# Optimization experiments

Measured on AMD Instinct MI355X. Metric: run time of the kernel, lower is better.

## Reference

```python
import jax, jax.numpy as jnp
import numpy as np

NL = 4   # numLayers (modules are shared across layers)
H = 8    # numSignalHeads; contextAttention has embed_dim=1 with 1 head


def _ln(x, g, b, eps=1e-10):
    m = x.mean(-1, keepdims=True)
    v = ((x - m) ** 2).mean(-1, keepdims=True)
    return (x - m) / jnp.sqrt(v + eps) * g + b


def _forward(signalData, contextualData, Ws, bs, bn_g, bn_b,
             cWq, cWk, cWv, cbq, cbk, cbv, cbias_k, cbias_v, cWo, cbo,
             xWq, xWk, xWv, xbq, xbk, xbv, xbias_k, xbias_v, xWo, xbo,
             W1, b1, W2, b2, W3, b3,
             ln_ff_g, ln_ff_b, ln_cas_g, ln_cas_b, ln_fin_g, ln_fin_b):
    B, S, E = signalData.shape
    dh = E // H
    scale = float(1.0 / np.sqrt(dh))
    # synthesizeContext: Linear(C,18) + BatchNorm1d(18, track_running_stats=False -> batch stats)
    ec = contextualData @ Ws.T + bs                       # (B,18)
    mu = ec.mean(0)
    var = ((ec - mu) ** 2).mean(0)                        # biased var (PyTorch BN)
    ec = (ec - mu) / jnp.sqrt(var + 1e-5) * bn_g + bn_b
    ec = ec[:, :, None]                                   # (B,18,1)
    sig = signalData
    for _ in range(NL):
        # --- self-attention on context: embed_dim=1, 1 head (head_dim=1, scale=1), add_bias_kv ---
        q = ec @ cWq.T + cbq                              # (B,18,1)
        k = jnp.concatenate([ec @ cWk.T + cbk, jnp.broadcast_to(cbias_k, (B, 1, 1))], axis=1)
        v = jnp.concatenate([ec @ cWv.T + cbv, jnp.broadcast_to(cbias_v, (B, 1, 1))], axis=1)
        a = jax.nn.softmax(jnp.einsum('bqd,bkd->bqk', q, k), axis=-1)
        sa = jnp.einsum('bqk,bkd->bqd', a, v) @ cWo.T + cbo
        ec = ec + sa
        # --- cross-attention: query/value = LN(signal) (E), key = context (kdim=1), add_bias_kv ---
        ns = _ln(sig, ln_cas_g, ln_cas_b)
        q = (ns @ xWq.T + xbq).reshape(B, S, H, dh)
        k = jnp.concatenate([ec @ xWk.T + xbk, jnp.broadcast_to(xbias_k, (B, 1, E))], axis=1).reshape(B, S + 1, H, dh)
        v = jnp.concatenate([ns @ xWv.T + xbv, jnp.broadcast_to(xbias_v, (B, 1, E))], axis=1).reshape(B, S + 1, H, dh)
        a = jax.nn.softmax(jnp.einsum('bqhd,bkhd->bhqk', q, k) * scale, axis=-1)
        ca = jnp.einsum('bhqk,bkhd->bqhd', a, v).reshape(B, S, E) @ xWo.T + xbo
        sig = sig + ca
        # --- feed-forward: Linear->SiLU->Linear->SiLU->Linear->SiLU (dropout = identity in eval) ---
        nf = _ln(sig, ln_ff_g, ln_ff_b)
        ff = jax.nn.silu(jax.nn.silu(jax.nn.silu(nf @ W1.T + b1) @ W2.T + b2) @ W3.T + b3)
        sig = sig + ff
    return _ln(sig, ln_fin_g, ln_fin_b)


def setup_inputs() -> dict:
    key = jax.random.key(0)
    ks = iter(jax.random.split(key, 48))
    r = lambda *s: jax.random.normal(next(ks), s, dtype=jnp.float32) * 0.05
    B, S, E, C = 4096, 18, 256, 512
    return dict(
        signalData=jax.random.normal(next(ks), (B, S, E), dtype=jnp.float32),
        contextualData=jax.random.normal(next(ks), (B, C), dtype=jnp.float32),
        Ws=r(18, C), bs=r(18), bn_g=jnp.ones(18, jnp.float32), bn_b=jnp.zeros(18, jnp.float32),
        cWq=r(1, 1), cWk=r(1, 1), cWv=r(1, 1), cbq=r(1), cbk=r(1), cbv=r(1),
        cbias_k=r(1), cbias_v=r(1), cWo=r(1, 1), cbo=r(1),
        xWq=r(E, E), xWk=r(E, 1), xWv=r(E, E), xbq=r(E), xbk=r(E), xbv=r(E),
        xbias_k=r(E), xbias_v=r(E), xWo=r(E, E), xbo=r(E),
        W1=r(32, E), b1=r(32), W2=r(16, 32), b2=r(16), W3=r(E, 16), b3=r(E),
        ln_ff_g=jnp.ones(E, jnp.float32), ln_ff_b=jnp.zeros(E, jnp.float32),
        ln_cas_g=jnp.ones(E, jnp.float32), ln_cas_b=jnp.zeros(E, jnp.float32),
        ln_fin_g=jnp.ones(E, jnp.float32), ln_fin_b=jnp.zeros(E, jnp.float32),
    )


def reference(signalData, contextualData, Ws, bs, bn_g, bn_b,
              cWq, cWk, cWv, cbq, cbk, cbv, cbias_k, cbias_v, cWo, cbo,
              xWq, xWk, xWv, xbq, xbk, xbv, xbias_k, xbias_v, xWo, xbo,
              W1, b1, W2, b2, W3, b3,
              ln_ff_g, ln_ff_b, ln_cas_g, ln_cas_b, ln_fin_g, ln_fin_b):
    return _forward(signalData, contextualData, Ws, bs, bn_g, bn_b,
                    cWq, cWk, cWv, cbq, cbk, cbv, cbias_k, cbias_v, cWo, cbo,
                    xWq, xWk, xWv, xbq, xbk, xbv, xbias_k, xbias_v, xWo, xbo,
                    W1, b1, W2, b2, W3, b3,
                    ln_ff_g, ln_ff_b, ln_cas_g, ln_cas_b, ln_fin_g, ln_fin_b)
```

## Files before the change

### kernel.cpp

```cpp
#include <hip/hip_runtime.h>

typedef unsigned short u16;
typedef __attribute__((ext_vector_type(8))) short bf16x8;
typedef __attribute__((ext_vector_type(4))) float f32x4;
typedef __attribute__((ext_vector_type(4))) unsigned int u32x4;
typedef __attribute__((ext_vector_type(2))) unsigned int u32x2;

#define MROWS 36
#define SWZ(r,c) ((c) ^ (((r)&7)<<3))

__device__ inline u16 f2bf(float f){
  unsigned int u = __float_as_uint(f);
  return (u16)((u + 0x7fffu + ((u>>16)&1u)) >> 16);
}
__device__ inline unsigned int packbf(float a, float b){
  return (unsigned int)f2bf(a) | ((unsigned int)f2bf(b)<<16);
}
__device__ inline float bfloat_lo(unsigned int u){ return __uint_as_float(u<<16); }
__device__ inline float bfloat_hi(unsigned int u){ return __uint_as_float(u & 0xffff0000u); }
__device__ inline float bf2f(u16 h){ return __uint_as_float(((unsigned int)h)<<16); }
__device__ inline float wred(float v){
  #pragma unroll
  for (int m=1;m<64;m<<=1) v += __shfl_xor(v, m, 64);
  return v;
}
__device__ inline float silu_f(float x){ return x / (1.f + __expf(-x)); }
__device__ inline f32x4 mfma16(bf16x8 a, bf16x8 b, f32x4 c){
  return __builtin_amdgcn_mfma_f32_16x16x32_bf16(a, b, c, 0, 0, 0);
}

struct Params {
  const float *sigIn;
  const float *bn_g, *bn_b;
  const float *cWq,*cWk,*cWv,*cbq,*cbk,*cbv,*cbias_k,*cbias_v,*cWo,*cbo;
  const float *xbv, *xbias_v, *xbo;
  const float *b1,*b2,*b3;
  const float *g_cas,*b_cas,*g_ff,*b_ff,*g_fin,*b_fin;
  const u16 *Wv,*Wo,*Wq3,*W1b,*W2b,*W3p;
  const float *bias3, *ecr, *mu, *rstd;
  float *out;
};

__global__ void k_prep(const float* __restrict__ xWq, const float* __restrict__ xWk,
                       const float* __restrict__ xWv, const float* __restrict__ xWo,
                       const float* __restrict__ xbq, const float* __restrict__ xbk,
                       const float* __restrict__ xbias_k,
                       const float* __restrict__ W1, const float* __restrict__ W2,
                       const float* __restrict__ W3,
                       u16* Wv, u16* Wo, u16* Wq3, u16* W1b, u16* W2b, u16* W3p, float* bias3){
  const int gid = blockIdx.x*blockDim.x + threadIdx.x;
  const int gsz = gridDim.x*blockDim.x;
  for (int i=gid;i<65536;i+=gsz) Wv[i]=f2bf(xWv[i]);
  for (int i=gid;i<65536;i+=gsz) Wo[i]=f2bf(xWo[i]);
  for (int i=gid;i<8192;i+=gsz)  W1b[i]=f2bf(W1[i]);
  for (int i=gid;i<512;i+=gsz)   W2b[i]=f2bf(W2[i]);
  for (int i=gid;i<8192;i+=gsz){ int o=i>>5, k=i&31; W3p[i] = (k<16)? f2bf(W3[o*16+k]) : (u16)0; }
  for (int i=gid;i<8192;i+=gsz){
    int r=i>>8, c=i&255;
    u16 outv = 0;
    if (r<24){
      int h=r&7, sel=r>>3;
      const float* vec = sel==0? xWk : (sel==1? xbk : xbias_k);
      float s=0.f;
      for (int d=0;d<32;++d) s += xWq[(size_t)(h*32+d)*256+c]*vec[h*32+d];
      outv = f2bf(s);
    }
    Wq3[i]=outv;
  }
  for (int i=gid;i<24;i+=gsz){
    int h=i&7, sel=i>>3;
    const float* vec = sel==0? xWk : (sel==1? xbk : xbias_k);
    float s=0.f; for (int d=0;d<32;++d) s += xbq[h*32+d]*vec[h*32+d];
    bias3[i]=s;
  }
}

__global__ void k_ec(const float* __restrict__ ctx, const float* __restrict__ Ws,
                     const float* __restrict__ bs, float* __restrict__ ecr){
  const int wave = threadIdx.x>>6, lane = threadIdx.x&63;
  const int b = blockIdx.x*4 + wave;
  const float* c = ctx + (size_t)b*512 + lane*8;
  const float4 a0 = *(const float4*)c, a1 = *(const float4*)(c+4);
  float cv[8] = {a0.x,a0.y,a0.z,a0.w,a1.x,a1.y,a1.z,a1.w};
  #pragma unroll 1
  for (int j=0;j<18;++j){
    const float* w = Ws + j*512 + lane*8;
    const float4 w0 = *(const float4*)w, w1 = *(const float4*)(w+4);
    float s = cv[0]*w0.x + cv[1]*w0.y + cv[2]*w0.z + cv[3]*w0.w
            + cv[4]*w1.x + cv[5]*w1.y + cv[6]*w1.z + cv[7]*w1.w;
    s = wred(s);
    if (lane==0) ecr[(size_t)b*18 + j] = s + bs[j];
  }
}

__global__ void k_bn(const float* __restrict__ ecr, float* __restrict__ mu, float* __restrict__ rstd){
  __shared__ float red[256];
  const int tid = threadIdx.x;
  for (int j=0;j<18;++j){
    float s=0.f, s2=0.f;
    for (int b=tid;b<4096;b+=256){ float v = ecr[(size_t)b*18+j]; s+=v; s2+=v*v; }
    red[tid]=s; __syncthreads();
    for (int o=128;o>0;o>>=1){ if(tid<o) red[tid]+=red[tid+o]; __syncthreads(); }
    float S = red[0]; __syncthreads();
    red[tid]=s2; __syncthreads();
    for (int o=128;o>0;o>>=1){ if(tid<o) red[tid]+=red[tid+o]; __syncthreads(); }
    float S2 = red[0]; __syncthreads();
    if (tid==0){ float m = S*(1.f/4096.f); float v = S2*(1.f/4096.f) - m*m;
                 mu[j]=m; rstd[j]=rsqrtf(v+1e-5f); }
  }
}

__global__ __launch_bounds__(256, 2) void k_main(Params P){
  __shared__ __attribute__((aligned(16))) u16 s_sig[MROWS][256];
  __shared__ __attribute__((aligned(16))) u16 s_ns [MROWS][256];
  __shared__ __attribute__((aligned(16))) u16 s_v  [MROWS][256];
  __shared__ __attribute__((aligned(16))) u16 s_h1 [MROWS][32];
  __shared__ float s_qq[MROWS][24];
  __shared__ float s_ec[2][18];

  const int tid  = threadIdx.x;
  const int wave = tid >> 6;
  const int lane = tid & 63;
  const int lr   = lane & 15;
  const int lkg  = lane >> 4;
  const int kof  = lkg * 8;
  const int dr   = lkg * 4;
  const int b0   = blockIdx.x * 2;

  for (int idx = tid*8; idx < MROWS*256; idx += 256*8){
    const int row = idx >> 8, col = idx & 255;
    const float* src = P.sigIn + ((size_t)b0*18 + row)*256 + col;
    const float4 a = *(const float4*)src;
    const float4 b = *(const float4*)(src+4);
    u32x4 w;
    w[0]=packbf(a.x,a.y); w[1]=packbf(a.z,a.w);
    w[2]=packbf(b.x,b.y); w[3]=packbf(b.z,b.w);
    *(u32x4*)&s_sig[row][SWZ(row,col)] = w;
  }
  if (tid < 36){
    const int nb = tid/18, j = tid - nb*18;
    const float raw = P.ecr[(size_t)(b0+nb)*18 + j];
    s_ec[nb][j] = (raw - P.mu[j]) * P.rstd[j] * P.bn_g[j] + P.bn_b[j];
  }
  __syncthreads();

  auto ln_pass = [&](const float* g, const float* bvec){
    #pragma unroll 1
    for (int r = wave*9; r < wave*9+9; ++r){
      const int col = lane*4;
      const u32x2 raw = *(const u32x2*)&s_sig[r][SWZ(r,col)];
      const float x0 = bfloat_lo(raw[0]), x1 = bfloat_hi(raw[0]);
      const float x2 = bfloat_lo(raw[1]), x3 = bfloat_hi(raw[1]);
      const float m = wred(x0+x1+x2+x3)*(1.f/256.f);
      const float d0=x0-m, d1=x1-m, d2=x2-m, d3=x3-m;
      const float rs = rsqrtf(wred(d0*d0+d1*d1+d2*d2+d3*d3)*(1.f/256.f)+1e-10f);
      const float4 gv = *(const float4*)(g+col);
      const float4 bv = *(const float4*)(bvec+col);
      u32x2 o;
      o[0] = packbf(d0*rs*gv.x+bv.x, d1*rs*gv.y+bv.y);
      o[1] = packbf(d2*rs*gv.z+bv.z, d3*rs*gv.w+bv.w);
      *(u32x2*)&s_ns[r][SWZ(r,col)] = o;
    }
  };

  for (int layer = 0; layer < 4; ++layer){
    float newec = 0.f;
    if (tid < 36){
      const int nb = tid/18, i = tid - nb*18;
      const float cwq=P.cWq[0], cbq=P.cbq[0], cwk=P.cWk[0], cbk=P.cbk[0];
      const float cwv=P.cWv[0], cbv=P.cbv[0], ck1=P.cbias_k[0], cv1=P.cbias_v[0];
      const float cwo=P.cWo[0], cbo=P.cbo[0];
      const float qi = s_ec[nb][i]*cwq + cbq;
      float sc[19]; float mx = -1e30f;
      #pragma unroll
      for (int j=0;j<18;++j){ sc[j] = qi*(s_ec[nb][j]*cwk + cbk); mx = fmaxf(mx, sc[j]); }
      sc[18] = qi*ck1; mx = fmaxf(mx, sc[18]);
      float den=0.f, o=0.f;
      #pragma unroll
      for (int j=0;j<18;++j){ const float pp=__expf(sc[j]-mx); den+=pp; o+=pp*(s_ec[nb][j]*cwv+cbv); }
      const float pp=__expf(sc[18]-mx); den+=pp; o+=pp*cv1;
      newec = s_ec[nb][i] + (o/den)*cwo + cbo;
    }
    __syncthreads();
    if (tid < 36){ const int nb = tid/18; s_ec[nb][tid - nb*18] = newec; }

    ln_pass(P.g_cas, P.b_cas);
    __syncthreads();

    {
      f32x4 accV[3][4]; f32x4 accQ[3];
      #pragma unroll
      for (int mt=0;mt<3;++mt){
        accQ[mt] = f32x4{0.f,0.f,0.f,0.f};
        #pragma unroll
        for (int nt=0;nt<4;++nt) accV[mt][nt] = f32x4{0.f,0.f,0.f,0.f};
      }
      for (int kk=0; kk<8; ++kk){
        const int k0 = kk*32 + kof;
        bf16x8 afr[3];
        #pragma unroll
        for (int mt=0;mt<3;++mt){
          const int row = mt*16 + lr;
          u32x4 raw = u32x4{0u,0u,0u,0u};
          if (row < MROWS) raw = *(const u32x4*)&s_ns[row][SWZ(row,k0)];
          afr[mt] = __builtin_bit_cast(bf16x8, raw);
        }
        #pragma unroll
        for (int nt=0;nt<4;++nt){
          const int n = (wave*4+nt)*16 + lr;
          const bf16x8 bfr = __builtin_bit_cast(bf16x8, *(const u32x4*)(P.Wv + (size_t)n*256 + k0));
          #pragma unroll
          for (int mt=0;mt<3;++mt) accV[mt][nt] = mfma16(afr[mt], bfr, accV[mt][nt]);
        }
        if (wave < 2){
          const bf16x8 bq = __builtin_bit_cast(bf16x8, *(const u32x4*)(P.Wq3 + (size_t)(wave*16+lr)*256 + k0));
          #pragma unroll
          for (int mt=0;mt<3;++mt) accQ[mt] = mfma16(afr[mt], bq, accQ[mt]);
        }
      }
      #pragma unroll
      for (int nt=0;nt<4;++nt){
        const int n = (wave*4+nt)*16 + lr;
        const float bias = P.xbv[n];
        #pragma unroll
        for (int mt=0;mt<3;++mt){
          #pragma unroll
          for (int q=0;q<4;++q){
            const int row = mt*16 + dr + q;
            if (row < MROWS) s_v[row][SWZ(row,n)] = f2bf(accV[mt][nt][q] + bias);
          }
        }
      }
      if (wave < 2){
        const int c = wave*16 + lr;
        if (c < 24){
          const float bias = P.bias3[c];
          #pragma unroll
          for (int mt=0;mt<3;++mt){
            #pragma unroll
            for (int q=0;q<4;++q){
              const int row = mt*16 + dr + q;
              if (row < MROWS) s_qq[row][c] = accQ[mt][q] + bias;
            }
          }
        }
      }
    }
    __syncthreads();

    {
      const float scale = 0.17677669529663687f;
      for (int t = tid; t < 288; t += 256){
        const int nb = t/144, rr = t - nb*144, h = rr/18, i = rr - h*18;
        const int qrow = nb*18 + i;
        const float qw = s_qq[qrow][h], qb = s_qq[qrow][8+h], q2v = s_qq[qrow][16+h];
        const float s18 = scale*q2v;
        float p[18]; float mx = s18;
        #pragma unroll
        for (int j=0;j<18;++j){ p[j] = scale*(s_ec[nb][j]*qw + qb); mx = fmaxf(mx, p[j]); }
        float den = 0.f;
        #pragma unroll
        for (int j=0;j<18;++j){ p[j] = __expf(p[j]-mx); den += p[j]; }
        const float p18 = __expf(s18-mx); den += p18;
        float acc[32];
        #pragma unroll
        for (int d4=0; d4<8; ++d4){
          const float4 xv = *(const float4*)(P.xbias_v + h*32 + d4*4);
          acc[d4*4+0]=p18*xv.x; acc[d4*4+1]=p18*xv.y; acc[d4*4+2]=p18*xv.z; acc[d4*4+3]=p18*xv.w;
        }
        #pragma unroll 1
        for (int j=0;j<18;++j){
          const float pj = p[j];
          const int vrow = nb*18 + j;
          #pragma unroll
          for (int d8=0; d8<4; ++d8){
            const u32x4 u = *(const u32x4*)&s_v[vrow][SWZ(vrow, h*32+d8*8)];
            #pragma unroll
            for (int q=0;q<4;++q){
              acc[d8*8+q*2]   += pj*bfloat_lo(u[q]);
              acc[d8*8+q*2+1] += pj*bfloat_hi(u[q]);
            }
          }
        }
        const float inv = 1.f/den;
        #pragma unroll
        for (int d8=0; d8<4; ++d8){
          u32x4 w;
          #pragma unroll
          for (int q=0;q<4;++q) w[q] = packbf(acc[d8*8+q*2]*inv, acc[d8*8+q*2+1]*inv);
          *(u32x4*)&s_ns[qrow][SWZ(qrow, h*32+d8*8)] = w;
        }
      }
    }
    __syncthreads();

    {
      f32x4 acc[3][4];
      #pragma unroll
      for (int mt=0;mt<3;++mt){
        #pragma unroll
        for (int nt=0;nt<4;++nt) acc[mt][nt] = f32x4{0.f,0.f,0.f,0.f};
      }
      for (int kk=0; kk<8; ++kk){
        const int k0 = kk*32 + kof;
        bf16x8 afr[3];
        #pragma unroll
        for (int mt=0;mt<3;++mt){
          const int row = mt*16 + lr;
          u32x4 raw = u32x4{0u,0u,0u,0u};
          if (row < MROWS) raw = *(const u32x4*)&s_ns[row][SWZ(row,k0)];
          afr[mt] = __builtin_bit_cast(bf16x8, raw);
        }
        #pragma unroll
        for (int nt=0;nt<4;++nt){
          const int n = (wave*4+nt)*16 + lr;
          const bf16x8 bfr = __builtin_bit_cast(bf16x8, *(const u32x4*)(P.Wo + (size_t)n*256 + k0));
          #pragma unroll
          for (int mt=0;mt<3;++mt) acc[mt][nt] = mfma16(afr[mt], bfr, acc[mt][nt]);
        }
      }
      #pragma unroll
      for (int nt=0;nt<4;++nt){
        const int n = (wave*4+nt)*16 + lr;
        const float bias = P.xbo[n];
        #pragma unroll
        for (int mt=0;mt<3;++mt){
          #pragma unroll
          for (int q=0;q<4;++q){
            const int row = mt*16 + dr + q;
            if (row < MROWS){
              const int si = SWZ(row,n);
              s_sig[row][si] = f2bf(bf2f(s_sig[row][si]) + acc[mt][nt][q] + bias);
            }
          }
        }
      }
    }
    __syncthreads();

    ln_pass(P.g_ff, P.b_ff);
    __syncthreads();

    if (wave < 2){
      f32x4 acc[3];
      #pragma unroll
      for (int mt=0;mt<3;++mt) acc[mt] = f32x4{0.f,0.f,0.f,0.f};
      for (int kk=0; kk<8; ++kk){
        const int k0 = kk*32 + kof;
        bf16x8 afr[3];
        #pragma unroll
        for (int mt=0;mt<3;++mt){
          const int row = mt*16 + lr;
          u32x4 raw = u32x4{0u,0u,0u,0u};
          if (row < MROWS) raw = *(const u32x4*)&s_ns[row][SWZ(row,k0)];
          afr[mt] = __builtin_bit_cast(bf16x8, raw);
        }
        const bf16x8 bfr = __builtin_bit_cast(bf16x8, *(const u32x4*)(P.W1b + (size_t)(wave*16+lr)*256 + k0));
        #pragma unroll
        for (int mt=0;mt<3;++mt) acc[mt] = mfma16(afr[mt], bfr, acc[mt]);
      }
      const int c = wave*16 + lr;
      const float bias = P.b1[c];
      #pragma unroll
      for (int mt=0;mt<3;++mt){
        #pragma unroll
        for (int q=0;q<4;++q){
          const int row = mt*16 + dr + q;
          if (row < MROWS) s_h1[row][c] = f2bf(silu_f(acc[mt][q] + bias));
        }
      }
    }
    __syncthreads();

    if (wave < 3){
      const int row_a = wave*16 + lr;
      u32x4 raw = u32x4{0u,0u,0u,0u};
      if (row_a < MROWS) raw = *(const u32x4*)&s_h1[row_a][kof];
      const bf16x8 a = __builtin_bit_cast(bf16x8, raw);
      const bf16x8 b = __builtin_bit_cast(bf16x8, *(const u32x4*)(P.W2b + (size_t)lr*32 + kof));
      f32x4 acc = mfma16(a, b, f32x4{0.f,0.f,0.f,0.f});
      const float bias = P.b2[lr];
      #pragma unroll
      for (int q=0;q<4;++q){
        const int row = wave*16 + dr + q;
        if (row < MROWS){
          s_h1[row][lr]    = f2bf(silu_f(acc[q] + bias));
          s_h1[row][lr+16] = 0;
        }
      }
    }
    __syncthreads();

    {
      bf16x8 afr[3];
      #pragma unroll
      for (int mt=0;mt<3;++mt){
        const int row = mt*16 + lr;
        u32x4 raw = u32x4{0u,0u,0u,0u};
        if (row < MROWS) raw = *(const u32x4*)&s_h1[row][kof];
        afr[mt] = __builtin_bit_cast(bf16x8, raw);
      }
      f32x4 acc[3][4];
      #pragma unroll
      for (int nt=0;nt<4;++nt){
        const int n = (wave*4+nt)*16 + lr;
        const bf16x8 bfr = __builtin_bit_cast(bf16x8, *(const u32x4*)(P.W3p + (size_t)n*32 + kof));
        #pragma unroll
        for (int mt=0;mt<3;++mt) acc[mt][nt] = mfma16(afr[mt], bfr, f32x4{0.f,0.f,0.f,0.f});
      }
      #pragma unroll
      for (int nt=0;nt<4;++nt){
        const int n = (wave*4+nt)*16 + lr;
        const float b3v = P.b3[n];
        #pragma unroll
        for (int mt=0;mt<3;++mt){
          #pragma unroll
          for (int q=0;q<4;++q){
            const int row = mt*16 + dr + q;
            if (row < MROWS){
              const int si = SWZ(row,n);
              s_sig[row][si] = f2bf(bf2f(s_sig[row][si]) + silu_f(acc[mt][nt][q] + b3v));
            }
          }
        }
      }
    }
    __syncthreads();
  }

  {
    #pragma unroll 1
    for (int r = wave*9; r < wave*9+9; ++r){
      const int col = lane*4;
      const u32x2 raw = *(const u32x2*)&s_sig[r][SWZ(r,col)];
      const float x0 = bfloat_lo(raw[0]), x1 = bfloat_hi(raw[0]);
      const float x2 = bfloat_lo(raw[1]), x3 = bfloat_hi(raw[1]);
      const float m = wred(x0+x1+x2+x3)*(1.f/256.f);
      const float d0=x0-m, d1=x1-m, d2=x2-m, d3=x3-m;
      const float rs = rsqrtf(wred(d0*d0+d1*d1+d2*d2+d3*d3)*(1.f/256.f)+1e-10f);
      const float4 gv = *(const float4*)(P.g_fin+col);
      const float4 bv = *(const float4*)(P.b_fin+col);
      float4 o;
      o.x = d0*rs*gv.x+bv.x; o.y = d1*rs*gv.y+bv.y;
      o.z = d2*rs*gv.z+bv.z; o.w = d3*rs*gv.w+bv.w;
      *(float4*)(P.out + ((size_t)b0*18 + r)*256 + col) = o;
    }
  }
}

extern "C" void kernel_launch(void* const* d_in, const int* in_sizes, int n_in,
                              void* d_out, int out_size, void* d_ws, size_t ws_size,
                              hipStream_t stream) {
  (void)in_sizes; (void)n_in; (void)out_size; (void)ws_size;
  const float* sigIn   = (const float*)d_in[0];
  const float* ctx     = (const float*)d_in[1];
  const float* Ws      = (const float*)d_in[2];
  const float* bs      = (const float*)d_in[3];
  const float* bn_g    = (const float*)d_in[4];
  const float* bn_b    = (const float*)d_in[5];
  const float* cWq     = (const float*)d_in[6];
  const float* cWk     = (const float*)d_in[7];
  const float* cWv     = (const float*)d_in[8];
  const float* cbq     = (const float*)d_in[9];
  const float* cbk     = (const float*)d_in[10];
  const float* cbv     = (const float*)d_in[11];
  const float* cbias_k = (const float*)d_in[12];
  const float* cbias_v = (const float*)d_in[13];
  const float* cWo     = (const float*)d_in[14];
  const float* cbo     = (const float*)d_in[15];
  const float* xWq     = (const float*)d_in[16];
  const float* xWk     = (const float*)d_in[17];
  const float* xWv     = (const float*)d_in[18];
  const float* xbq     = (const float*)d_in[19];
  const float* xbk     = (const float*)d_in[20];
  const float* xbv     = (const float*)d_in[21];
  const float* xbias_k = (const float*)d_in[22];
  const float* xbias_v = (const float*)d_in[23];
  const float* xWo     = (const float*)d_in[24];
  const float* xbo     = (const float*)d_in[25];
  const float* W1      = (const float*)d_in[26];
  const float* b1      = (const float*)d_in[27];
  const float* W2      = (const float*)d_in[28];
  const float* b2      = (const float*)d_in[29];
  const float* W3      = (const float*)d_in[30];
  const float* b3      = (const float*)d_in[31];
  const float* g_ff    = (const float*)d_in[32];
  const float* b_ff    = (const float*)d_in[33];
  const float* g_cas   = (const float*)d_in[34];
  const float* b_cas   = (const float*)d_in[35];
  const float* g_fin   = (const float*)d_in[36];
  const float* b_fin   = (const float*)d_in[37];

  char* ws = (char*)d_ws;
  u16*  Wv    = (u16*)(ws);
  u16*  Wo    = (u16*)(ws + 131072);
  u16*  Wq3   = (u16*)(ws + 262144);
  u16*  W1b   = (u16*)(ws + 278528);
  u16*  W2b   = (u16*)(ws + 294912);
  u16*  W3p   = (u16*)(ws + 295936);
  float* bias3= (float*)(ws + 312320);
  float* ecr  = (float*)(ws + 312448);
  float* mu   = (float*)(ws + 607360);
  float* rstd = (float*)(ws + 607488);

  k_prep<<<dim3(64), dim3(256), 0, stream>>>(xWq, xWk, xWv, xWo, xbq, xbk, xbias_k,
                                             W1, W2, W3, Wv, Wo, Wq3, W1b, W2b, W3p, bias3);
  k_ec<<<dim3(1024), dim3(256), 0, stream>>>(ctx, Ws, bs, ecr);
  k_bn<<<dim3(1), dim3(256), 0, stream>>>(ecr, mu, rstd);

  Params P;
  P.sigIn = sigIn; P.bn_g = bn_g; P.bn_b = bn_b;
  P.cWq=cWq; P.cWk=cWk; P.cWv=cWv; P.cbq=cbq; P.cbk=cbk; P.cbv=cbv;
  P.cbias_k=cbias_k; P.cbias_v=cbias_v; P.cWo=cWo; P.cbo=cbo;
  P.xbv=xbv; P.xbias_v=xbias_v; P.xbo=xbo;
  P.b1=b1; P.b2=b2; P.b3=b3;
  P.g_cas=g_cas; P.b_cas=b_cas; P.g_ff=g_ff; P.b_ff=b_ff; P.g_fin=g_fin; P.b_fin=b_fin;
  P.Wv=Wv; P.Wo=Wo; P.Wq3=Wq3; P.W1b=W1b; P.W2b=W2b; P.W3p=W3p;
  P.bias3=bias3; P.ecr=ecr; P.mu=mu; P.rstd=rstd;
  P.out = (float*)d_out;

  k_main<<<dim3(2048), dim3(256), 0, stream>>>(P);
}
```

Baseline: 850.7 us.

## Process one batch element per block instead of two, doubling grid size

Each block now handles a single batch element (18 rows) instead of two (36 rows), and the grid doubles to 4096 blocks with launch bounds raised to 4 blocks per CU. The M dimension of the MFMA tiles shrinks from 3 to 2 tiles of 16, and the attention loop becomes a single 144-thread pass. This halves LDS per block and aims for higher occupancy and less serialized work per block. The cost is more padded MFMA work per useful row (18 rows in 32) and each block reloading the weight fragments from global memory.

```diff
diff --git a/kernel.cpp b/kernel.cpp
--- a/kernel.cpp
+++ b/kernel.cpp
@@ -6,7 +6,8 @@
 typedef __attribute__((ext_vector_type(4))) unsigned int u32x4;
 typedef __attribute__((ext_vector_type(2))) unsigned int u32x2;
 
-#define MROWS 36
+#define MROWS 18
+#define MT 2
 #define SWZ(r,c) ((c) ^ (((r)&7)<<3))
 
 __device__ inline u16 f2bf(float f){
@@ -110,13 +111,13 @@
   }
 }
 
-__global__ __launch_bounds__(256, 2) void k_main(Params P){
+__global__ __launch_bounds__(256, 4) void k_main(Params P){
   __shared__ __attribute__((aligned(16))) u16 s_sig[MROWS][256];
   __shared__ __attribute__((aligned(16))) u16 s_ns [MROWS][256];
   __shared__ __attribute__((aligned(16))) u16 s_v  [MROWS][256];
   __shared__ __attribute__((aligned(16))) u16 s_h1 [MROWS][32];
   __shared__ float s_qq[MROWS][24];
-  __shared__ float s_ec[2][18];
+  __shared__ float s_ec[MROWS];
 
   const int tid  = threadIdx.x;
   const int wave = tid >> 6;
@@ -125,7 +126,7 @@
   const int lkg  = lane >> 4;
   const int kof  = lkg * 8;
   const int dr   = lkg * 4;
-  const int b0   = blockIdx.x * 2;
+  const int b0   = blockIdx.x;
 
   for (int idx = tid*8; idx < MROWS*256; idx += 256*8){
     const int row = idx >> 8, col = idx & 255;
@@ -137,16 +138,14 @@
     w[2]=packbf(b.x,b.y); w[3]=packbf(b.z,b.w);
     *(u32x4*)&s_sig[row][SWZ(row,col)] = w;
   }
-  if (tid < 36){
-    const int nb = tid/18, j = tid - nb*18;
-    const float raw = P.ecr[(size_t)(b0+nb)*18 + j];
-    s_ec[nb][j] = (raw - P.mu[j]) * P.rstd[j] * P.bn_g[j] + P.bn_b[j];
+  if (tid < MROWS){
+    const float raw = P.ecr[(size_t)b0*18 + tid];
+    s_ec[tid] = (raw - P.mu[tid]) * P.rstd[tid] * P.bn_g[tid] + P.bn_b[tid];
   }
   __syncthreads();
 
   auto ln_pass = [&](const float* g, const float* bvec){
-    #pragma unroll 1
-    for (int r = wave*9; r < wave*9+9; ++r){
+    for (int r = wave; r < MROWS; r += 4){
       const int col = lane*4;
       const u32x2 raw = *(const u32x2*)&s_sig[r][SWZ(r,col)];
       const float x0 = bfloat_lo(raw[0]), x1 = bfloat_hi(raw[0]);
@@ -165,41 +164,41 @@
 
   for (int layer = 0; layer < 4; ++layer){
     float newec = 0.f;
-    if (tid < 36){
-      const int nb = tid/18, i = tid - nb*18;
+    if (tid < MROWS){
+      const int i = tid;
       const float cwq=P.cWq[0], cbq=P.cbq[0], cwk=P.cWk[0], cbk=P.cbk[0];
       const float cwv=P.cWv[0], cbv=P.cbv[0], ck1=P.cbias_k[0], cv1=P.cbias_v[0];
       const float cwo=P.cWo[0], cbo=P.cbo[0];
-      const float qi = s_ec[nb][i]*cwq + cbq;
+      const float qi = s_ec[i]*cwq + cbq;
       float sc[19]; float mx = -1e30f;
       #pragma unroll
-      for (int j=0;j<18;++j){ sc[j] = qi*(s_ec[nb][j]*cwk + cbk); mx = fmaxf(mx, sc[j]); }
+      for (int j=0;j<18;++j){ sc[j] = qi*(s_ec[j]*cwk + cbk); mx = fmaxf(mx, sc[j]); }
       sc[18] = qi*ck1; mx = fmaxf(mx, sc[18]);
       float den=0.f, o=0.f;
       #pragma unroll
-      for (int j=0;j<18;++j){ const float pp=__expf(sc[j]-mx); den+=pp; o+=pp*(s_ec[nb][j]*cwv+cbv); }
+      for (int j=0;j<18;++j){ const float pp=__expf(sc[j]-mx); den+=pp; o+=pp*(s_ec[j]*cwv+cbv); }
       const float pp=__expf(sc[18]-mx); den+=pp; o+=pp*cv1;
-      newec = s_ec[nb][i] + (o/den)*cwo + cbo;
-    }
-    __syncthreads();
-    if (tid < 36){ const int nb = tid/18; s_ec[nb][tid - nb*18] = newec; }
+      newec = s_ec[i] + (o/den)*cwo + cbo;
+    }
+    __syncthreads();
+    if (tid < MROWS) s_ec[tid] = newec;
 
     ln_pass(P.g_cas, P.b_cas);
     __syncthreads();
 
     {
-      f32x4 accV[3][4]; f32x4 accQ[3];
-      #pragma unroll
-      for (int mt=0;mt<3;++mt){
+      f32x4 accV[MT][4]; f32x4 accQ[MT];
+      #pragma unroll
+      for (int mt=0;mt<MT;++mt){
         accQ[mt] = f32x4{0.f,0.f,0.f,0.f};
         #pragma unroll
         for (int nt=0;nt<4;++nt) accV[mt][nt] = f32x4{0.f,0.f,0.f,0.f};
       }
       for (int kk=0; kk<8; ++kk){
         const int k0 = kk*32 + kof;
-        bf16x8 afr[3];
-        #pragma unroll
-        for (int mt=0;mt<3;++mt){
+        bf16x8 afr[MT];
+        #pragma unroll
+        for (int mt=0;mt<MT;++mt){
           const int row = mt*16 + lr;
           u32x4 raw = u32x4{0u,0u,0u,0u};
           if (row < MROWS) raw = *(const u32x4*)&s_ns[row][SWZ(row,k0)];
@@ -210,12 +209,12 @@
           const int n = (wave*4+nt)*16 + lr;
           const bf16x8 bfr = __builtin_bit_cast(bf16x8, *(const u32x4*)(P.Wv + (size_t)n*256 + k0));
           #pragma unroll
-          for (int mt=0;mt<3;++mt) accV[mt][nt] = mfma16(afr[mt], bfr, accV[mt][nt]);
+          for (int mt=0;mt<MT;++mt) accV[mt][nt] = mfma16(afr[mt], bfr, accV[mt][nt]);
         }
         if (wave < 2){
           const bf16x8 bq = __builtin_bit_cast(bf16x8, *(const u32x4*)(P.Wq3 + (size_t)(wave*16+lr)*256 + k0));
           #pragma unroll
-          for (int mt=0;mt<3;++mt) accQ[mt] = mfma16(afr[mt], bq, accQ[mt]);
+          for (int mt=0;mt<MT;++mt) accQ[mt] = mfma16(afr[mt], bq, accQ[mt]);
         }
       }
       #pragma unroll
@@ -223,7 +222,7 @@
         const int n = (wave*4+nt)*16 + lr;
         const float bias = P.xbv[n];
         #pragma unroll
-        for (int mt=0;mt<3;++mt){
+        for (int mt=0;mt<MT;++mt){
           #pragma unroll
           for (int q=0;q<4;++q){
             const int row = mt*16 + dr + q;
@@ -236,7 +235,7 @@
         if (c < 24){
           const float bias = P.bias3[c];
           #pragma unroll
-          for (int mt=0;mt<3;++mt){
+          for (int mt=0;mt<MT;++mt){
             #pragma unroll
             for (int q=0;q<4;++q){
               const int row = mt*16 + dr + q;
@@ -248,64 +247,60 @@
     }
     __syncthreads();
 
+    if (tid < 144){
+      const float scale = 0.17677669529663687f;
+      const int h = tid/18, i = tid - h*18;
+      const float qw = s_qq[i][h], qb = s_qq[i][8+h], q2v = s_qq[i][16+h];
+      const float s18 = scale*q2v;
+      float p[18]; float mx = s18;
+      #pragma unroll
+      for (int j=0;j<18;++j){ p[j] = scale*(s_ec[j]*qw + qb); mx = fmaxf(mx, p[j]); }
+      float den = 0.f;
+      #pragma unroll
+      for (int j=0;j<18;++j){ p[j] = __expf(p[j]-mx); den += p[j]; }
+      const float p18 = __expf(s18-mx); den += p18;
+      float acc[32];
+      #pragma unroll
+      for (int d4=0; d4<8; ++d4){
+        const float4 xv = *(const float4*)(P.xbias_v + h*32 + d4*4);
+        acc[d4*4+0]=p18*xv.x; acc[d4*4+1]=p18*xv.y; acc[d4*4+2]=p18*xv.z; acc[d4*4+3]=p18*xv.w;
+      }
+      #pragma unroll 1
+      for (int j=0;j<18;++j){
+        const float pj = p[j];
+        #pragma unroll
+        for (int d8=0; d8<4; ++d8){
+          const u32x4 u = *(const u32x4*)&s_v[j][SWZ(j, h*32+d8*8)];
+          #pragma unroll
+          for (int q=0;q<4;++q){
+            acc[d8*8+q*2]   += pj*bfloat_lo(u[q]);
+            acc[d8*8+q*2+1] += pj*bfloat_hi(u[q]);
+          }
+        }
+      }
+      const float inv = 1.f/den;
+      #pragma unroll
+      for (int d8=0; d8<4; ++d8){
+        u32x4 w;
+        #pragma unroll
+        for (int q=0;q<4;++q) w[q] = packbf(acc[d8*8+q*2]*inv, acc[d8*8+q*2+1]*inv);
+        *(u32x4*)&s_ns[i][SWZ(i, h*32+d8*8)] = w;
+      }
+    }
+    __syncthreads();
+
     {
-      const float scale = 0.17677669529663687f;
-      for (int t = tid; t < 288; t += 256){
-        const int nb = t/144, rr = t - nb*144, h = rr/18, i = rr - h*18;
-        const int qrow = nb*18 + i;
-        const float qw = s_qq[qrow][h], qb = s_qq[qrow][8+h], q2v = s_qq[qrow][16+h];
-        const float s18 = scale*q2v;
-        float p[18]; float mx = s18;
-        #pragma unroll
-        for (int j=0;j<18;++j){ p[j] = scale*(s_ec[nb][j]*qw + qb); mx = fmaxf(mx, p[j]); }
-        float den = 0.f;
-        #pragma unroll
-        for (int j=0;j<18;++j){ p[j] = __expf(p[j]-mx); den += p[j]; }
-        const float p18 = __expf(s18-mx); den += p18;
-        float acc[32];
-        #pragma unroll
-        for (int d4=0; d4<8; ++d4){
-          const float4 xv = *(const float4*)(P.xbias_v + h*32 + d4*4);
-          acc[d4*4+0]=p18*xv.x; acc[d4*4+1]=p18*xv.y; acc[d4*4+2]=p18*xv.z; acc[d4*4+3]=p18*xv.w;
-        }
-        #pragma unroll 1
-        for (int j=0;j<18;++j){
-          const float pj = p[j];
-          const int vrow = nb*18 + j;
-          #pragma unroll
-          for (int d8=0; d8<4; ++d8){
-            const u32x4 u = *(const u32x4*)&s_v[vrow][SWZ(vrow, h*32+d8*8)];
-            #pragma unroll
-            for (int q=0;q<4;++q){
-              acc[d8*8+q*2]   += pj*bfloat_lo(u[q]);
-              acc[d8*8+q*2+1] += pj*bfloat_hi(u[q]);
-            }
-          }
-        }
-        const float inv = 1.f/den;
-        #pragma unroll
-        for (int d8=0; d8<4; ++d8){
-          u32x4 w;
-          #pragma unroll
-          for (int q=0;q<4;++q) w[q] = packbf(acc[d8*8+q*2]*inv, acc[d8*8+q*2+1]*inv);
-          *(u32x4*)&s_ns[qrow][SWZ(qrow, h*32+d8*8)] = w;
-        }
-      }
-    }
-    __syncthreads();
-
-    {
-      f32x4 acc[3][4];
-      #pragma unroll
-      for (int mt=0;mt<3;++mt){
+      f32x4 acc[MT][4];
+      #pragma unroll
+      for (int mt=0;mt<MT;++mt){
         #pragma unroll
         for (int nt=0;nt<4;++nt) acc[mt][nt] = f32x4{0.f,0.f,0.f,0.f};
       }
       for (int kk=0; kk<8; ++kk){
         const int k0 = kk*32 + kof;
-        bf16x8 afr[3];
-        #pragma unroll
-        for (int mt=0;mt<3;++mt){
+        bf16x8 afr[MT];
+        #pragma unroll
+        for (int mt=0;mt<MT;++mt){
           const int row = mt*16 + lr;
           u32x4 raw = u32x4{0u,0u,0u,0u};
           if (row < MROWS) raw = *(const u32x4*)&s_ns[row][SWZ(row,k0)];
@@ -316,7 +311,7 @@
           const int n = (wave*4+nt)*16 + lr;
           const bf16x8 bfr = __builtin_bit_cast(bf16x8, *(const u32x4*)(P.Wo + (size_t)n*256 + k0));
           #pragma unroll
-          for (int mt=0;mt<3;++mt) acc[mt][nt] = mfma16(afr[mt], bfr, acc[mt][nt]);
+          for (int mt=0;mt<MT;++mt) acc[mt][nt] = mfma16(afr[mt], bfr, acc[mt][nt]);
         }
       }
       #pragma unroll
@@ -324,7 +319,7 @@
         const int n = (wave*4+nt)*16 + lr;
         const float bias = P.xbo[n];
         #pragma unroll
-        for (int mt=0;mt<3;++mt){
+        for (int mt=0;mt<MT;++mt){
           #pragma unroll
           for (int q=0;q<4;++q){
             const int row = mt*16 + dr + q;
@@ -342,14 +337,14 @@
     __syncthreads();
 
     if (wave < 2){
-      f32x4 acc[3];
-      #pragma unroll
-      for (int mt=0;mt<3;++mt) acc[mt] = f32x4{0.f,0.f,0.f,0.f};
+      f32x4 acc[MT];
+      #pragma unroll
+      for (int mt=0;mt<MT;++mt) acc[mt] = f32x4{0.f,0.f,0.f,0.f};
       for (int kk=0; kk<8; ++kk){
         const int k0 = kk*32 + kof;
-        bf16x8 afr[3];
-        #pragma unroll
-        for (int mt=0;mt<3;++mt){
+        bf16x8 afr[MT];
+        #pragma unroll
+        for (int mt=0;mt<MT;++mt){
           const int row = mt*16 + lr;
           u32x4 raw = u32x4{0u,0u,0u,0u};
           if (row < MROWS) raw = *(const u32x4*)&s_ns[row][SWZ(row,k0)];
@@ -357,12 +352,12 @@
         }
         const bf16x8 bfr = __builtin_bit_cast(bf16x8, *(const u32x4*)(P.W1b + (size_t)(wave*16+lr)*256 + k0));
         #pragma unroll
-        for (int mt=0;mt<3;++mt) acc[mt] = mfma16(afr[mt], bfr, acc[mt]);
+        for (int mt=0;mt<MT;++mt) acc[mt] = mfma16(afr[mt], bfr, acc[mt]);
       }
       const int c = wave*16 + lr;
       const float bias = P.b1[c];
       #pragma unroll
-      for (int mt=0;mt<3;++mt){
+      for (int mt=0;mt<MT;++mt){
         #pragma unroll
         for (int q=0;q<4;++q){
           const int row = mt*16 + dr + q;
@@ -372,7 +367,7 @@
     }
     __syncthreads();
 
-    if (wave < 3){
+    if (wave < MT){
       const int row_a = wave*16 + lr;
       u32x4 raw = u32x4{0u,0u,0u,0u};
       if (row_a < MROWS) raw = *(const u32x4*)&s_h1[row_a][kof];
@@ -392,28 +387,28 @@
     __syncthreads();
 
     {
-      bf16x8 afr[3];
-      #pragma unroll
-      for (int mt=0;mt<3;++mt){
+      bf16x8 afr[MT];
+      #pragma unroll
+      for (int mt=0;mt<MT;++mt){
         const int row = mt*16 + lr;
         u32x4 raw = u32x4{0u,0u,0u,0u};
         if (row < MROWS) raw = *(const u32x4*)&s_h1[row][kof];
         afr[mt] = __builtin_bit_cast(bf16x8, raw);
       }
-      f32x4 acc[3][4];
+      f32x4 acc[MT][4];
       #pragma unroll
       for (int nt=0;nt<4;++nt){
         const int n = (wave*4+nt)*16 + lr;
         const bf16x8 bfr = __builtin_bit_cast(bf16x8, *(const u32x4*)(P.W3p + (size_t)n*32 + kof));
         #pragma unroll
-        for (int mt=0;mt<3;++mt) acc[mt][nt] = mfma16(afr[mt], bfr, f32x4{0.f,0.f,0.f,0.f});
+        for (int mt=0;mt<MT;++mt) acc[mt][nt] = mfma16(afr[mt], bfr, f32x4{0.f,0.f,0.f,0.f});
       }
       #pragma unroll
       for (int nt=0;nt<4;++nt){
         const int n = (wave*4+nt)*16 + lr;
         const float b3v = P.b3[n];
         #pragma unroll
-        for (int mt=0;mt<3;++mt){
+        for (int mt=0;mt<MT;++mt){
           #pragma unroll
           for (int q=0;q<4;++q){
             const int row = mt*16 + dr + q;
@@ -429,8 +424,7 @@
   }
 
   {
-    #pragma unroll 1
-    for (int r = wave*9; r < wave*9+9; ++r){
+    for (int r = wave; r < MROWS; r += 4){
       const int col = lane*4;
       const u32x2 raw = *(const u32x2*)&s_sig[r][SWZ(r,col)];
       const float x0 = bfloat_lo(raw[0]), x1 = bfloat_hi(raw[0]);
@@ -519,5 +513,5 @@
   P.bias3=bias3; P.ecr=ecr; P.mu=mu; P.rstd=rstd;
   P.out = (float*)d_out;
 
-  k_main<<<dim3(2048), dim3(256), 0, stream>>>(P);
-}
+  k_main<<<dim3(4096), dim3(256), 0, stream>>>(P);
+}
```

Result: slower. 1.193 ms (+40.2%).
